# Optimization experiments

Hardware: AMD Instinct MI355X
Metric: run time of the kernel (lower is better)

## Reference

```python
import jax, jax.numpy as jnp
import numpy as np

# q4_0: blocks of 32 weights; per block: 2-byte fp16 scale 'd' + 16 packed bytes
# (element i in low nibble of byte i, element i+16 in high nibble). value = d*(q-8).
SHAPE = (8192, 8192)
NUMEL = SHAPE[0] * SHAPE[1]
QK = 32
NBLOCKS = NUMEL // QK          # 2_097_152
BLOCK_BYTES = 18               # 2 (fp16 scale) + 16 (packed nibbles)


def setup_inputs() -> dict:
    rng = np.random.default_rng(0)
    w = (rng.standard_normal((NBLOCKS, QK)) * 0.02).astype(np.float32)
    # faithful q4_0 requantization (ggml): d = signed max-magnitude value / -8
    amax_idx = np.argmax(np.abs(w), axis=1)
    maxv = w[np.arange(NBLOCKS), amax_idx]
    d = (maxv / -8.0).astype(np.float16)
    inv_d = np.where(d != 0, 1.0 / d.astype(np.float32), 0.0)
    q = np.clip(np.rint(w * inv_d[:, None]) + 8.0, 0, 15).astype(np.uint8)
    packed = (q[:, :16] | (q[:, 16:] << 4)).astype(np.uint8)     # [NB,16]
    scale_bytes = d.view(np.uint8).reshape(NBLOCKS, 2)            # little-endian fp16 bits
    raw = np.concatenate([scale_bytes, packed], axis=1).reshape(-1)  # [NB*18] uint8
    return {"raw_data": jnp.asarray(raw)}


def reference(raw_data) -> jnp.ndarray:
    raw = raw_data.reshape(NBLOCKS, BLOCK_BYTES)
    # reassemble fp16 scale from two little-endian bytes
    s16 = raw[:, 0].astype(jnp.uint16) | (raw[:, 1].astype(jnp.uint16) << 8)
    scale = jax.lax.bitcast_convert_type(s16, jnp.float16).astype(jnp.float32)  # [NB]
    qs = raw[:, 2:]                                   # [NB,16] packed nibbles
    lo = (qs & 0xF).astype(jnp.float32)               # elements 0..15
    hi = (qs >> 4).astype(jnp.float32)                # elements 16..31
    q = jnp.concatenate([lo, hi], axis=1) - 8.0       # [NB,32]
    return (scale[:, None] * q).reshape(SHAPE)
```

## Files before the change

### kernel.cpp

```cpp
#include <hip/hip_runtime.h>
#include <hip/hip_fp16.h>


constexpr long long NUMEL = 8192LL * 8192LL;
constexpr int QK = 32;
constexpr long long NBLOCKS = NUMEL / QK;
constexpr int BLOCK_INTS = 18;
constexpr int WG_BLOCKS = 32;
constexpr int WG_INTS = WG_BLOCKS * BLOCK_INTS;

__global__ __launch_bounds__(256)
void dequant_q4_kernel(const int* __restrict__ raw32,
                       float4* __restrict__ out4)
{
    __shared__ int lds[WG_INTS];

    const int tid = threadIdx.x;
    const long long wg = blockIdx.x;

    if (tid < WG_INTS / 4) {
        const int4 v = *(const int4*)(raw32 + wg * WG_INTS + (long long)tid * 4);
        ((int4*)lds)[tid] = v;
    }
    __syncthreads();

    const int bl = tid >> 3;
    const int k  = tid & 7;
    const int base = bl * BLOCK_INTS;

    const int2 s = *(const int2*)(lds + base);
    const unsigned short s16 = (unsigned short)((s.x & 0xff) | ((s.y & 0xff) << 8));
    const float scale = __half2float(__ushort_as_half(s16));

    const int j = (k & 3) * 4;
    const int2 q01 = *(const int2*)(lds + base + 2 + j);
    const int2 q23 = *(const int2*)(lds + base + 4 + j);

    const int sh = (k >= 4) ? 4 : 0;

    float4 o;
    o.x = scale * (float)(((q01.x >> sh) & 15) - 8);
    o.y = scale * (float)(((q01.y >> sh) & 15) - 8);
    o.z = scale * (float)(((q23.x >> sh) & 15) - 8);
    o.w = scale * (float)(((q23.y >> sh) & 15) - 8);

    out4[wg * 256 + tid] = o;
}

extern "C" void kernel_launch(void* const* d_in, const int* in_sizes, int n_in,
                              void* d_out, int out_size, void* d_ws, size_t ws_size,
                              hipStream_t stream)
{
    const int* raw32 = (const int*)d_in[0];
    float4* out4 = (float4*)d_out;

    const long long n_wg = NBLOCKS / WG_BLOCKS;
    dequant_q4_kernel<<<dim3((unsigned)n_wg), dim3(256), 0, stream>>>(raw32, out4);
}
```

Before: 353.4 us.

## Process four times more blocks per workgroup with nontemporal loads and stores

```diff
diff --git a/kernel.cpp b/kernel.cpp
--- a/kernel.cpp
+++ b/kernel.cpp
@@ -1,50 +1,64 @@
 #include <hip/hip_runtime.h>
 #include <hip/hip_fp16.h>
 
+
+typedef int   i4 __attribute__((ext_vector_type(4)));
+typedef int   i2 __attribute__((ext_vector_type(2)));
+typedef float f4 __attribute__((ext_vector_type(4)));
 
 constexpr long long NUMEL = 8192LL * 8192LL;
 constexpr int QK = 32;
 constexpr long long NBLOCKS = NUMEL / QK;
 constexpr int BLOCK_INTS = 18;
-constexpr int WG_BLOCKS = 32;
+constexpr int WG_BLOCKS = 128;
 constexpr int WG_INTS = WG_BLOCKS * BLOCK_INTS;
+constexpr int WG_INT4 = WG_INTS / 4;
 
 __global__ __launch_bounds__(256)
 void dequant_q4_kernel(const int* __restrict__ raw32,
-                       float4* __restrict__ out4)
+                       f4* __restrict__ out4)
 {
-    __shared__ int lds[WG_INTS];
+    __shared__ __align__(16) int lds[WG_INTS];
 
     const int tid = threadIdx.x;
     const long long wg = blockIdx.x;
 
-    if (tid < WG_INTS / 4) {
-        const int4 v = *(const int4*)(raw32 + wg * WG_INTS + (long long)tid * 4);
-        ((int4*)lds)[tid] = v;
-    }
+    const i4* __restrict__ src = (const i4*)(raw32 + wg * (long long)WG_INTS);
+    i4* lds4 = (i4*)lds;
+
+    lds4[tid]       = __builtin_nontemporal_load(src + tid);
+    lds4[tid + 256] = __builtin_nontemporal_load(src + tid + 256);
+    if (tid < WG_INT4 - 512)
+        lds4[tid + 512] = __builtin_nontemporal_load(src + tid + 512);
+
     __syncthreads();
 
-    const int bl = tid >> 3;
     const int k  = tid & 7;
-    const int base = bl * BLOCK_INTS;
+    const int j  = (k & 3) * 4;
+    const int sh = (k >= 4) ? 4 : 0;
+    const int c  = tid >> 3;
+    const long long outbase = wg * (long long)(WG_BLOCKS * 8) + tid;
 
-    const int2 s = *(const int2*)(lds + base);
-    const unsigned short s16 = (unsigned short)((s.x & 0xff) | ((s.y & 0xff) << 8));
-    const float scale = __half2float(__ushort_as_half(s16));
+#pragma unroll
+    for (int r = 0; r < 4; ++r) {
+        const int base = (c + r * 32) * BLOCK_INTS;
 
-    const int j = (k & 3) * 4;
-    const int2 q01 = *(const int2*)(lds + base + 2 + j);
-    const int2 q23 = *(const int2*)(lds + base + 4 + j);
+        const i2 s = *(const i2*)(lds + base);
+        const unsigned short s16 =
+            (unsigned short)((s.x & 0xff) | ((s.y & 0xff) << 8));
+        const float scale = __half2float(__ushort_as_half(s16));
 
-    const int sh = (k >= 4) ? 4 : 0;
+        const i2 q01 = *(const i2*)(lds + base + 2 + j);
+        const i2 q23 = *(const i2*)(lds + base + 4 + j);
 
-    float4 o;
-    o.x = scale * (float)(((q01.x >> sh) & 15) - 8);
-    o.y = scale * (float)(((q01.y >> sh) & 15) - 8);
-    o.z = scale * (float)(((q23.x >> sh) & 15) - 8);
-    o.w = scale * (float)(((q23.y >> sh) & 15) - 8);
+        f4 o;
+        o.x = scale * (float)(((q01.x >> sh) & 15) - 8);
+        o.y = scale * (float)(((q01.y >> sh) & 15) - 8);
+        o.z = scale * (float)(((q23.x >> sh) & 15) - 8);
+        o.w = scale * (float)(((q23.y >> sh) & 15) - 8);
 
-    out4[wg * 256 + tid] = o;
+        __builtin_nontemporal_store(o, out4 + outbase + r * 256);
+    }
 }
 
 extern "C" void kernel_launch(void* const* d_in, const int* in_sizes, int n_in,
@@ -52,7 +66,7 @@
                               hipStream_t stream)
 {
     const int* raw32 = (const int*)d_in[0];
-    float4* out4 = (float4*)d_out;
+    f4* out4 = (f4*)d_out;
 
     const long long n_wg = NBLOCKS / WG_BLOCKS;
     dequant_q4_kernel<<<dim3((unsigned)n_wg), dim3(256), 0, stream>>>(raw32, out4);
```

New measurement: 353.9 us. About the same (+0.1%).
